# Kernel tuning notes

Measured on AMD Instinct MI355X. Metric: run time of the kernel, lower is better.

Reference implementation:

```python
import jax, jax.numpy as jnp
import numpy as np

B, DIM, H, N, M = 2, 256, 4, 4096, 4096
DH = DIM // H  # per-head dim
EPS = 1e-5


def conv1(x, W, b):
    # kernel_size=1 Conv1d == channel-wise linear: x [B,Cin,N], W [Cin,Cout]
    return jnp.einsum('bin,io->bon', x, W) + b[None, :, None]


def setup_inputs() -> dict:
    key = jax.random.key(0)
    ks = jax.random.split(key, 12)
    s = lambda fan: 1.0 / np.sqrt(fan)
    return {
        'x': jax.random.normal(ks[0], (B, DIM, N), jnp.float32),
        'source': jax.random.normal(ks[1], (B, DIM, M), jnp.float32),
        'Wq': jax.random.normal(ks[2], (DIM, DIM), jnp.float32) * s(DIM),
        'bq': jax.random.normal(ks[3], (DIM,), jnp.float32) * 0.01,
        'Wk': jax.random.normal(ks[4], (DIM, DIM), jnp.float32) * s(DIM),
        'bk': jax.random.normal(ks[5], (DIM,), jnp.float32) * 0.01,
        'Wv': jax.random.normal(ks[6], (DIM, DIM), jnp.float32) * s(DIM),
        'bv': jax.random.normal(ks[7], (DIM,), jnp.float32) * 0.01,
        'Wo': jax.random.normal(ks[8], (DIM, DIM), jnp.float32) * s(DIM),
        'bo': jax.random.normal(ks[9], (DIM,), jnp.float32) * 0.01,
        'W1': jax.random.normal(ks[10], (2 * DIM, 2 * DIM), jnp.float32) * s(2 * DIM),
        'b1': jnp.zeros((2 * DIM,), jnp.float32),
        'gamma': jnp.ones((2 * DIM,), jnp.float32),
        'beta': jnp.zeros((2 * DIM,), jnp.float32),
        'W2': jax.random.normal(ks[11], (2 * DIM, DIM), jnp.float32) * s(2 * DIM),
        'b2': jnp.zeros((DIM,), jnp.float32),
    }


def reference(x, source, Wq, bq, Wk, bk, Wv, bv, Wo, bo, W1, b1, gamma, beta, W2, b2):
    b = x.shape[0]
    # projections, then split channels as (d_head, heads): view(B, DH, H, L)
    q = conv1(x, Wq, bq).reshape(b, DH, H, -1)       # [B,DH,H,N]
    k = conv1(source, Wk, bk).reshape(b, DH, H, -1)  # [B,DH,H,M]
    v = conv1(source, Wv, bv).reshape(b, DH, H, -1)  # [B,DH,H,M]
    scores = jnp.einsum('bdhn,bdhm->bhnm', q, k) / np.sqrt(DH)  # [B,H,N,M]
    p = jax.nn.softmax(scores, axis=-1)
    attn = jnp.einsum('bhnm,bdhm->bdhn', p, v)        # [B,DH,H,N]
    message = conv1(attn.reshape(b, DIM, -1), Wo, bo)  # [B,DIM,N]
    h = conv1(jnp.concatenate([x, message], axis=1), W1, b1)  # [B,2DIM,N]
    # BatchNorm1d in train mode: batch stats over (batch, length)
    mean = jnp.mean(h, axis=(0, 2), keepdims=True)
    var = jnp.var(h, axis=(0, 2), keepdims=True)
    h = (h - mean) * jax.lax.rsqrt(var + EPS)
    h = h * gamma[None, :, None] + beta[None, :, None]
    h = jax.nn.relu(h)
    return conv1(h, W2, b2)  # [B,DIM,N]
```

## Files before the change

### kernel.cpp

```cpp
#include <hip/hip_runtime.h>
#include <hip/hip_bf16.h>
#include <math.h>

#define NB   2
#define DIM  256
#define NH   4
#define DH   64
#define LEN  4096
#define EPSBN 1e-5f
#define QSC  0.18033688f

typedef __attribute__((ext_vector_type(8))) short bf16x8;
typedef __attribute__((ext_vector_type(4))) float f32x4;
typedef __attribute__((ext_vector_type(16))) float f32x16;
typedef __attribute__((ext_vector_type(4))) unsigned short u16x4;
typedef unsigned short ushortT;

__device__ __forceinline__ unsigned short f2bf(float f) {
    unsigned int u = __float_as_uint(f);
    u += 0x7FFFu + ((u >> 16) & 1u);
    return (unsigned short)(u >> 16);
}
__device__ __forceinline__ float bf2f(unsigned short u) {
    return __uint_as_float(((unsigned int)u) << 16);
}
__device__ __forceinline__ unsigned int cvtpk_bf16(float lo, float hi) {
    unsigned int r;
    asm volatile("v_cvt_pk_bf16_f32 %0, %1, %2" : "=v"(r) : "v"(lo), "v"(hi));
    return r;
}
__device__ __forceinline__ float sum16(const f32x16& v) {
    float s01 = v[0] + v[1], s23 = v[2] + v[3], s45 = v[4] + v[5], s67 = v[6] + v[7];
    float s89 = v[8] + v[9], sab = v[10] + v[11], scd = v[12] + v[13], sef = v[14] + v[15];
    return ((s01 + s23) + (s45 + s67)) + ((s89 + sab) + (scd + sef));
}
#define MFMA(a, b, c)   __builtin_amdgcn_mfma_f32_16x16x32_bf16((a), (b), (c), 0, 0, 0)
#define MFMA32(a, b, c) __builtin_amdgcn_mfma_f32_32x32x16_bf16((a), (b), (c), 0, 0, 0)

__global__ __launch_bounds__(256)
void prep_all(const float* __restrict__ x, const float* __restrict__ src,
              const float* __restrict__ Wq, const float* __restrict__ Wk,
              const float* __restrict__ Wv, const float* __restrict__ Wo,
              const float* __restrict__ W1, const float* __restrict__ W2,
              const float* __restrict__ bq, const float* __restrict__ bk,
              const float* __restrict__ bv, const float* __restrict__ bo,
              const float* __restrict__ b1v,
              ushortT* WqT, ushortT* WkT, ushortT* WvT,
              ushortT* W1fT, ushortT* W2T,
              float* bqs, float* bks, float* bvs, float* bfused,
              ushortT* __restrict__ xT, ushortT* __restrict__ srcT)
{
    const int y = blockIdx.y;
    const int idx = blockIdx.x * 256 + threadIdx.x;
    const int t = threadIdx.x;
    if (y <= 2) {
        if (idx < 65536) {
            int op = idx >> 8, i = idx & 255;
            int o = (op & 63) * 4 + (op >> 6);
            if (y == 0)      WqT[idx] = f2bf(Wq[i * 256 + o] * QSC);
            else if (y == 1) WkT[idx] = f2bf(Wk[i * 256 + o]);
            else             WvT[idx] = f2bf(Wv[i * 256 + o]);
        }
    } else if (y == 3) {
        int o = idx >> 9, i = idx & 511;
        if (i < 256) W1fT[o * 512 + i] = f2bf(W1[i * 512 + o]);
    } else if (y == 4) {
        if (idx < 131072) { int o = idx >> 9, i = idx & 511; W2T[idx] = f2bf(W2[i * 256 + o]); }
    } else if (y == 5) {
        if (blockIdx.x == 0 && idx < 256) {
            int o = (idx & 63) * 4 + (idx >> 6);
            bqs[idx] = bq[o] * QSC;
            bks[idx] = bk[o];
            bvs[idx] = bv[o];
        }
    } else if (y <= 7) {
        const int bid = blockIdx.x + (y - 6) * 1024;
        const int c0 = (bid & 31) * 8;
        const int n0 = ((bid >> 5) & 15) * 256;
        const int z = bid >> 9;
        const int b = z & 1;
        const float* in = (z >> 1) ? src : x;
        ushortT* out = (z >> 1) ? srcT : xT;
        const int n = n0 + t;
        bf16x8 v;
#pragma unroll
        for (int j = 0; j < 8; ++j)
            v[j] = (short)f2bf(in[(((b << 8) + c0 + j) << 12) + n]);
        *(bf16x8*)&out[(((b << 12) + n) << 8) + c0] = v;
    } else {
        if (blockIdx.x >= 40) return;
        const int oy = blockIdx.x / 5, xi = blockIdx.x % 5;
        __shared__ float red[4][64];
        if (xi == 4) {
            const int part = t >> 6, oo = t & 63;
            const int o = oy * 64 + oo;
            float s = 0.f;
            for (int c = part * 64; c < part * 64 + 64; ++c)
                s += bo[c] * W1[(256 + c) * 512 + o];
            red[part][oo] = s;
            __syncthreads();
            if (part == 0)
                bfused[o] = ((red[0][oo] + red[1][oo]) + (red[2][oo] + red[3][oo])) + b1v[o];
            return;
        }
        const int w = t >> 6, l2 = t & 63, lg = l2 >> 4, ll = l2 & 15;
        const int wr = w >> 1, wc = w & 1;
        const int a0t = xi * 64, o0 = oy * 64;
        const int oA = o0 + wr * 32;
        const int aB = a0t + wc * 32;
        f32x4 acc[2][2] = {};
        const int ra = aB + ll, rb = aB + 16 + ll;
        const int r0 = (ra & 63) * 4 + (ra >> 6);
        const int r1 = (rb & 63) * 4 + (rb >> 6);
#pragma unroll
        for (int kk = 0; kk < 256; kk += 32) {
            const int cbase = 256 + kk + lg * 8;
            bf16x8 a0, a1;
#pragma unroll
            for (int j = 0; j < 8; ++j) {
                a0[j] = (short)f2bf(W1[(size_t)(cbase + j) * 512 + oA + ll]);
                a1[j] = (short)f2bf(W1[(size_t)(cbase + j) * 512 + oA + 16 + ll]);
            }
            const float* p0 = Wo + r0 * 256 + kk + lg * 8;
            const float* p1 = Wo + r1 * 256 + kk + lg * 8;
            float4 f00 = *(const float4*)p0, f01 = *(const float4*)(p0 + 4);
            float4 f10 = *(const float4*)p1, f11 = *(const float4*)(p1 + 4);
            bf16x8 b0, b1;
            b0[0] = (short)f2bf(f00.x); b0[1] = (short)f2bf(f00.y);
            b0[2] = (short)f2bf(f00.z); b0[3] = (short)f2bf(f00.w);
            b0[4] = (short)f2bf(f01.x); b0[5] = (short)f2bf(f01.y);
            b0[6] = (short)f2bf(f01.z); b0[7] = (short)f2bf(f01.w);
            b1[0] = (short)f2bf(f10.x); b1[1] = (short)f2bf(f10.y);
            b1[2] = (short)f2bf(f10.z); b1[3] = (short)f2bf(f10.w);
            b1[4] = (short)f2bf(f11.x); b1[5] = (short)f2bf(f11.y);
            b1[6] = (short)f2bf(f11.z); b1[7] = (short)f2bf(f11.w);
            acc[0][0] = MFMA(a0, b0, acc[0][0]);
            acc[0][1] = MFMA(a0, b1, acc[0][1]);
            acc[1][0] = MFMA(a1, b0, acc[1][0]);
            acc[1][1] = MFMA(a1, b1, acc[1][1]);
        }
#pragma unroll
        for (int f = 0; f < 2; ++f)
#pragma unroll
            for (int g = 0; g < 2; ++g) {
                const int ap = aB + g * 16 + ll;
#pragma unroll
                for (int r = 0; r < 4; ++r) {
                    const int o = oA + f * 16 + lg * 4 + r;
                    W1fT[o * 512 + 256 + ap] = f2bf(acc[f][g][r]);
                }
            }
    }
}

#define GEMM_STAGE(AROWP, BROWP)                                              \
    {                                                                         \
        _Pragma("unroll")                                                     \
        for (int i_ = 0; i_ < 4; ++i_) {                                      \
            const int row_ = i_ * 32 + srow;                                  \
            bf16x8 va_ = *(const bf16x8*)(AROWP(row_) + sc8 * 8);             \
            bf16x8 vb_ = *(const bf16x8*)(BROWP(row_) + sc8 * 8);             \
            const int dst_ = (row_ * 8 + (sc8 ^ (row_ & 7))) * 8;             \
            *(bf16x8*)&ldsA[dst_] = va_;                                      \
            *(bf16x8*)&ldsB[dst_] = vb_;                                      \
        }                                                                     \
    }

#define GEMM_FRAGS(k2_)                                                       \
    bf16x8 af[4], bfr[4];                                                     \
    {                                                                         \
        _Pragma("unroll")                                                     \
        for (int fo_ = 0; fo_ < 4; ++fo_) {                                   \
            const int ra_ = wr * 64 + fo_ * 16 + ll;                          \
            af[fo_] = *(const bf16x8*)&ldsA[(ra_ * 8 + (((k2_) * 4 + lg) ^ (ra_ & 7))) * 8]; \
            const int rb_ = wc * 64 + fo_ * 16 + ll;                          \
            bfr[fo_] = *(const bf16x8*)&ldsB[(rb_ * 8 + (((k2_) * 4 + lg) ^ (rb_ & 7))) * 8]; \
        }                                                                     \
    }

#define GEMM_MFMA16()                                                         \
    _Pragma("unroll")                                                         \
    for (int fo_ = 0; fo_ < 4; ++fo_) {                                       \
        _Pragma("unroll")                                                     \
        for (int fn_ = 0; fn_ < 4; ++fn_)                                     \
            acc[fo_][fn_] = MFMA(af[fo_], bfr[fn_], acc[fo_][fn_]);           \
    }

__global__ __launch_bounds__(256)
void qkv128(const ushortT* __restrict__ xT, const ushortT* __restrict__ srcT,
            const ushortT* __restrict__ WqT, const ushortT* __restrict__ WkT,
            const ushortT* __restrict__ WvT,
            const float* __restrict__ bqs, const float* __restrict__ bks,
            const float* __restrict__ bvs,
            ushortT* __restrict__ QT, ushortT* __restrict__ KT,
            ushortT* __restrict__ Vb)
{
    __shared__ __align__(16) ushortT ldsA[8192];
    __shared__ __align__(16) ushortT ldsB[8192];
    const int z = blockIdx.z, sel = z >> 1, b = z & 1;
    const int t = threadIdx.x, w = t >> 6, l = t & 63, lg = l >> 4, ll = l & 15;
    const int wr = w >> 1, wc = w & 1;
    const int n0 = blockIdx.x * 128, o0 = blockIdx.y * 128;
    const int srow = t >> 3, sc8 = t & 7;

    const ushortT* Agl;
    const ushortT* Bgl;
    int Arb, Brb;
    if (sel == 0)      { Agl = WqT;  Arb = o0;              Bgl = xT;   Brb = (b << 12) + n0; }
    else if (sel == 1) { Agl = WkT;  Arb = o0;              Bgl = srcT; Brb = (b << 12) + n0; }
    else               { Agl = srcT; Arb = (b << 12) + n0;  Bgl = WvT;  Brb = o0; }

    f32x4 acc[4][4] = {};
#define AROW(r_) (Agl + (size_t)(Arb + (r_)) * 256 + kk)
#define BROW(r_) (Bgl + (size_t)(Brb + (r_)) * 256 + kk)
    for (int kk = 0; kk < 256; kk += 64) {
        GEMM_STAGE(AROW, BROW);
        __syncthreads();
#pragma unroll
        for (int k2 = 0; k2 < 2; ++k2) {
            GEMM_FRAGS(k2);
            GEMM_MFMA16();
        }
        __syncthreads();
    }
#undef AROW
#undef BROW

    if (sel < 2) {
        const float* bias = sel ? bks : bqs;
        ushortT* out = sel ? KT : QT;
#pragma unroll
        for (int f = 0; f < 4; ++f) {
            const int ob = o0 + wr * 64 + f * 16 + lg * 4;
            f32x4 bv = *(const f32x4*)&bias[ob];
            const int hh = ob >> 6, d = ob & 63;
#pragma unroll
            for (int g = 0; g < 4; ++g) {
                const int n = n0 + wc * 64 + g * 16 + ll;
                u16x4 pk;
#pragma unroll
                for (int r = 0; r < 4; ++r) pk[r] = f2bf(acc[f][g][r] + bv[r]);
                *(u16x4*)&out[((((b << 2) + hh) << 12) + n) * 64 + d] = pk;
            }
        }
    } else {
#pragma unroll
        for (int g = 0; g < 4; ++g) {
            const int op = o0 + wc * 64 + g * 16 + ll;
            const float bb = bvs[op];
            const int hh = op >> 6, d = op & 63;
#pragma unroll
            for (int f = 0; f < 4; ++f) {
                const int m = n0 + wr * 64 + f * 16 + lg * 4;
                u16x4 pk;
#pragma unroll
                for (int r = 0; r < 4; ++r) pk[r] = f2bf(acc[f][g][r] + bb);
                *(u16x4*)&Vb[((((b << 2) + hh) << 6) + d) * 4096 + m] = pk;
            }
        }
    }
}

__global__ __launch_bounds__(256)
void gemmh128(const ushortT* __restrict__ xT, const ushortT* __restrict__ attnT,
              const ushortT* __restrict__ W1fT, const float* __restrict__ bfused,
              ushortT* __restrict__ hT, float* __restrict__ Sp, float* __restrict__ SSp)
{
    __shared__ __align__(16) ushortT ldsA[8192];
    __shared__ __align__(16) ushortT ldsB[8192];
    const int t = threadIdx.x, w = t >> 6, l = t & 63, lg = l >> 4, ll = l & 15;
    const int wr = w >> 1, wc = w & 1;
    const int n0 = blockIdx.x * 128, o0 = blockIdx.y * 128, b = blockIdx.z;
    const int srow = t >> 3, sc8 = t & 7;

    f32x4 acc[4][4] = {};
    for (int kk = 0; kk < 512; kk += 64) {
        const ushortT* Bsrc = (kk < 256) ? xT : attnT;
        const int kb = kk & 255;
#define AROW(r_) (W1fT + (size_t)(o0 + (r_)) * 512 + kk)
#define BROW(r_) (Bsrc + (size_t)((b << 12) + n0 + (r_)) * 256 + kb)
        GEMM_STAGE(AROW, BROW);
#undef AROW
#undef BROW
        __syncthreads();
#pragma unroll
        for (int k2 = 0; k2 < 2; ++k2) {
            GEMM_FRAGS(k2);
            GEMM_MFMA16();
        }
        __syncthreads();
    }

#pragma unroll
    for (int f = 0; f < 4; ++f) {
        const int ob = o0 + wr * 64 + f * 16 + lg * 4;
        f32x4 bv = *(const f32x4*)&bfused[ob];
        f32x4 hv[4];
#pragma unroll
        for (int g = 0; g < 4; ++g) {
            const int n = n0 + wc * 64 + g * 16 + ll;
            u16x4 pk;
#pragma unroll
            for (int r = 0; r < 4; ++r) {
                hv[g][r] = acc[f][g][r] + bv[r];
                pk[r] = f2bf(hv[g][r]);
            }
            *(u16x4*)&hT[(((b << 12) + n) << 9) + ob] = pk;
        }
#pragma unroll
        for (int r = 0; r < 4; ++r) {
            float s  = (hv[0][r] + hv[1][r]) + (hv[2][r] + hv[3][r]);
            float q2 = (hv[0][r] * hv[0][r] + hv[1][r] * hv[1][r]) +
                       (hv[2][r] * hv[2][r] + hv[3][r] * hv[3][r]);
#pragma unroll
            for (int off = 1; off < 16; off <<= 1) {
                s  += __shfl_xor(s, off);
                q2 += __shfl_xor(q2, off);
            }
            if (ll == 0) {
                const int o = ob + r;
                const int pidx = (o * 2 + b) * 64 + blockIdx.x * 2 + wc;
                Sp[pidx] = s;
                SSp[pidx] = q2;
            }
        }
    }
}

__global__ __launch_bounds__(128)
void bn_fin2(const float* __restrict__ S, const float* __restrict__ SS,
             const float* __restrict__ gamma, const float* __restrict__ beta,
             float* __restrict__ scale, float* __restrict__ shift)
{
    const int c = blockIdx.x, t = threadIdx.x;
    float s = S[c * 128 + t];
    float ss = SS[c * 128 + t];
#pragma unroll
    for (int off = 32; off; off >>= 1) {
        s += __shfl_down(s, off);
        ss += __shfl_down(ss, off);
    }
    __shared__ float red[4];
    const int wid = t >> 6;
    if ((t & 63) == 0) { red[wid] = s; red[2 + wid] = ss; }
    __syncthreads();
    if (t == 0) {
        s = red[0] + red[1];
        ss = red[2] + red[3];
        const float cnt = (float)NB * (float)LEN;
        float mean = s / cnt;
        float var = ss / cnt - mean * mean;
        float sc = gamma[c] * rsqrtf(var + EPSBN);
        scale[c] = sc;
        shift[c] = beta[c] - mean * sc;
    }
}

__global__ __launch_bounds__(256)
void gemmw2_128(const ushortT* __restrict__ hT, const ushortT* __restrict__ W2T,
                const float* __restrict__ bias, const float* __restrict__ scale,
                const float* __restrict__ shift, float* __restrict__ out)
{
    __shared__ __align__(16) ushortT ldsA[8192];
    __shared__ __align__(16) ushortT ldsB[8192];
    const int t = threadIdx.x, w = t >> 6, l = t & 63, lg = l >> 4, ll = l & 15;
    const int wr = w >> 1, wc = w & 1;
    const int n0 = blockIdx.x * 128, o0 = blockIdx.y * 128, b = blockIdx.z;
    const int srow = t >> 3, sc8 = t & 7;

    f32x4 acc[4][4] = {};
    for (int kk = 0; kk < 512; kk += 64) {
#define AROW(r_) (W2T + (size_t)(o0 + (r_)) * 512 + kk)
#define BROW(r_) (hT + (size_t)((b << 12) + n0 + (r_)) * 512 + kk)
        GEMM_STAGE(AROW, BROW);
#undef AROW
#undef BROW
        __syncthreads();
#pragma unroll
        for (int k2 = 0; k2 < 2; ++k2) {
            GEMM_FRAGS(k2);
            const int ch = kk + k2 * 32 + lg * 8;
            f32x4 sc0 = *(const f32x4*)&scale[ch];
            f32x4 sc1 = *(const f32x4*)&scale[ch + 4];
            f32x4 sh0 = *(const f32x4*)&shift[ch];
            f32x4 sh1 = *(const f32x4*)&shift[ch + 4];
#pragma unroll
            for (int fn = 0; fn < 4; ++fn) {
                bf16x8 raw = bfr[fn], bb;
#pragma unroll
                for (int j = 0; j < 4; ++j) {
                    float v0 = fmaxf(bf2f((unsigned short)raw[j]) * sc0[j] + sh0[j], 0.f);
                    float v1 = fmaxf(bf2f((unsigned short)raw[j + 4]) * sc1[j] + sh1[j], 0.f);
                    bb[j] = (short)f2bf(v0);
                    bb[j + 4] = (short)f2bf(v1);
                }
                bfr[fn] = bb;
            }
            GEMM_MFMA16();
        }
        __syncthreads();
    }

#pragma unroll
    for (int f = 0; f < 4; ++f) {
        const int ob = o0 + wr * 64 + f * 16 + lg * 4;
        f32x4 bv = *(const f32x4*)&bias[ob];
#pragma unroll
        for (int g = 0; g < 4; ++g) {
            const int n = n0 + wc * 64 + g * 16 + ll;
#pragma unroll
            for (int r = 0; r < 4; ++r)
                out[(((b << 8) + ob + r) << 12) + n] = acc[f][g][r] + bv[r];
        }
    }
}

__global__ __launch_bounds__(256)
void attn9(const ushortT* __restrict__ QT, const ushortT* __restrict__ KT,
           const ushortT* __restrict__ Vg, ushortT* __restrict__ attnT)
{
    __shared__ __align__(16) float olds[6144];
    __shared__ float llds[192];
    const int t = threadIdx.x, w = t >> 6, l = t & 63;
    const int hi = l >> 5, ln = l & 31;
    const int f = blockIdx.x, bh = f & 7, nt = f >> 3;
    const int b = bh >> 2, h = bh & 3;
    const int n0 = nt * 64;

    bf16x8 qf[2][4];
#pragma unroll
    for (int qb = 0; qb < 2; ++qb) {
        const int qrow = ((bh << 12) + n0 + qb * 32 + ln) * 64 + hi * 8;
#pragma unroll
        for (int dblk = 0; dblk < 4; ++dblk)
            qf[qb][dblk] = *(const bf16x8*)&QT[qrow + dblk * 16];
    }

    f32x16 o[2][2] = {};
    float l_loc[2] = {0.f, 0.f};

    const ushortT* Kb0 = KT + ((bh << 12) + w * 32 + ln) * 64 + hi * 8;
    const ushortT* Vb0 = Vg + ((bh << 6) + ln) * 4096 + w * 32 + hi * 8;

#pragma unroll 1
    for (int s = 0; s < 32; ++s) {
        const ushortT* Kp = Kb0 + s * 128 * 64;
        f32x16 st0 = {}, st1 = {};
        {
            bf16x8 ka = *(const bf16x8*)(Kp);
            bf16x8 kb = *(const bf16x8*)(Kp + 16);
            __builtin_amdgcn_s_setprio(1);
            st0 = MFMA32(ka, qf[0][0], st0);
            st1 = MFMA32(ka, qf[1][0], st1);
            st0 = MFMA32(kb, qf[0][1], st0);
            st1 = MFMA32(kb, qf[1][1], st1);
            __builtin_amdgcn_s_setprio(0);
            ka = *(const bf16x8*)(Kp + 32);
            kb = *(const bf16x8*)(Kp + 48);
            __builtin_amdgcn_s_setprio(1);
            st0 = MFMA32(ka, qf[0][2], st0);
            st1 = MFMA32(ka, qf[1][2], st1);
            st0 = MFMA32(kb, qf[0][3], st0);
            st1 = MFMA32(kb, qf[1][3], st1);
            __builtin_amdgcn_s_setprio(0);
        }

#pragma unroll
        for (int r = 0; r < 16; ++r) st0[r] = __builtin_amdgcn_exp2f(st0[r]);
#pragma unroll
        for (int r = 0; r < 16; ++r) st1[r] = __builtin_amdgcn_exp2f(st1[r]);
        l_loc[0] += sum16(st0);
        l_loc[1] += sum16(st1);

        bf16x8 pb0[2], pb1[2];
        {
            unsigned int pk0[8], pk1[8];
#pragma unroll
            for (int j = 0; j < 8; ++j) {
                pk0[j] = cvtpk_bf16(st0[2 * j], st0[2 * j + 1]);
                pk1[j] = cvtpk_bf16(st1[2 * j], st1[2 * j + 1]);
            }
#pragma unroll
            for (int sb = 0; sb < 2; ++sb) {
                unsigned int a0 = pk0[4 * sb], b0 = pk0[4 * sb + 2];
                unsigned int a1 = pk0[4 * sb + 1], b1 = pk0[4 * sb + 3];
                asm volatile("v_permlane32_swap_b32 %0, %1" : "+v"(a0), "+v"(b0));
                asm volatile("v_permlane32_swap_b32 %0, %1" : "+v"(a1), "+v"(b1));
                union { unsigned int u[4]; bf16x8 v; } tp;
                tp.u[0] = a0; tp.u[1] = a1; tp.u[2] = b0; tp.u[3] = b1;
                pb0[sb] = tp.v;
                unsigned int c0 = pk1[4 * sb], d0 = pk1[4 * sb + 2];
                unsigned int c1 = pk1[4 * sb + 1], d1 = pk1[4 * sb + 3];
                asm volatile("v_permlane32_swap_b32 %0, %1" : "+v"(c0), "+v"(d0));
                asm volatile("v_permlane32_swap_b32 %0, %1" : "+v"(c1), "+v"(d1));
                union { unsigned int u[4]; bf16x8 v; } tq;
                tq.u[0] = c0; tq.u[1] = c1; tq.u[2] = d0; tq.u[3] = d1;
                pb1[sb] = tq.v;
            }
        }

        const ushortT* Vp = Vb0 + s * 128;
        {
            bf16x8 va = *(const bf16x8*)(Vp);
            bf16x8 vb = *(const bf16x8*)(Vp + 16);
            __builtin_amdgcn_s_setprio(1);
            o[0][0] = MFMA32(va, pb0[0], o[0][0]);
            o[1][0] = MFMA32(va, pb1[0], o[1][0]);
            o[0][0] = MFMA32(vb, pb0[1], o[0][0]);
            o[1][0] = MFMA32(vb, pb1[1], o[1][0]);
            __builtin_amdgcn_s_setprio(0);
            va = *(const bf16x8*)(Vp + 32 * 4096);
            vb = *(const bf16x8*)(Vp + 32 * 4096 + 16);
            __builtin_amdgcn_s_setprio(1);
            o[0][1] = MFMA32(va, pb0[0], o[0][1]);
            o[1][1] = MFMA32(va, pb1[0], o[1][1]);
            o[0][1] = MFMA32(vb, pb0[1], o[0][1]);
            o[1][1] = MFMA32(vb, pb1[1], o[1][1]);
            __builtin_amdgcn_s_setprio(0);
        }
    }

    float lw[2];
    lw[0] = l_loc[0] + __shfl_xor(l_loc[0], 32);
    lw[1] = l_loc[1] + __shfl_xor(l_loc[1], 32);
    if (w && hi == 0) {
        llds[(w - 1) * 64 + ln] = lw[0];
        llds[(w - 1) * 64 + 32 + ln] = lw[1];
    }
#pragma unroll
    for (int qb = 0; qb < 2; ++qb) {
        if (w) {
            const int base = (w - 1) * 2048 + l;
#pragma unroll
            for (int r = 0; r < 16; ++r) olds[base + r * 64] = o[qb][0][r];
#pragma unroll
            for (int r = 0; r < 16; ++r) olds[base + (16 + r) * 64] = o[qb][1][r];
        }
        __syncthreads();
        if (w == 0) {
#pragma unroll
            for (int j = 0; j < 3; ++j) {
                const int base = j * 2048 + l;
#pragma unroll
                for (int r = 0; r < 16; ++r) o[qb][0][r] += olds[base + r * 64];
#pragma unroll
                for (int r = 0; r < 16; ++r) o[qb][1][r] += olds[base + (16 + r) * 64];
            }
        }
        __syncthreads();
    }

    if (w == 0) {
        float li[2] = {lw[0], lw[1]};
#pragma unroll
        for (int j = 0; j < 3; ++j) {
            li[0] += llds[j * 64 + ln];
            li[1] += llds[j * 64 + 32 + ln];
        }
#pragma unroll
        for (int qb = 0; qb < 2; ++qb) {
            const float linv = 1.f / li[qb];
            ushortT* orow = attnT + ((((b << 12) + n0 + qb * 32 + ln)) << 8) + (h << 6);
#pragma unroll
            for (int j = 0; j < 8; ++j) {
                const int d0 = ((2 * j) & 3) + 8 * (j >> 1) + 4 * hi;
                *(unsigned int*)&orow[d0] =
                    cvtpk_bf16(o[qb][0][2 * j] * linv, o[qb][0][2 * j + 1] * linv);
                *(unsigned int*)&orow[32 + d0] =
                    cvtpk_bf16(o[qb][1][2 * j] * linv, o[qb][1][2 * j + 1] * linv);
            }
        }
    }
}

extern "C" void kernel_launch(void* const* d_in, const int* in_sizes, int n_in,
                              void* d_out, int out_size, void* d_ws, size_t ws_size,
                              hipStream_t stream)
{
    const float* x   = (const float*)d_in[0];
    const float* src = (const float*)d_in[1];
    const float* Wq  = (const float*)d_in[2];
    const float* bq  = (const float*)d_in[3];
    const float* Wk  = (const float*)d_in[4];
    const float* bk  = (const float*)d_in[5];
    const float* Wv  = (const float*)d_in[6];
    const float* bv  = (const float*)d_in[7];
    const float* Wo  = (const float*)d_in[8];
    const float* bo  = (const float*)d_in[9];
    const float* W1  = (const float*)d_in[10];
    const float* b1  = (const float*)d_in[11];
    const float* gam = (const float*)d_in[12];
    const float* bet = (const float*)d_in[13];
    const float* W2  = (const float*)d_in[14];
    const float* b2  = (const float*)d_in[15];
    float* outp = (float*)d_out;

    char* W = (char*)d_ws;
    ushortT* xT    = (ushortT*)(W);
    ushortT* srcT  = (ushortT*)(W + (4u << 20));
    ushortT* QT    = (ushortT*)(W + (8u << 20));
    ushortT* KT    = (ushortT*)(W + (12u << 20));
    ushortT* Vb    = (ushortT*)(W + (16u << 20));
    ushortT* attnT = (ushortT*)(W + (20u << 20));
    ushortT* hT    = KT;
    float* Sp  = (float*)(W + (8u << 20));
    float* SSp = (float*)(W + (9u << 20));
    char* WB = W + (24u << 20);
    ushortT* WqT  = (ushortT*)(WB);
    ushortT* WkT  = (ushortT*)(WB + (128u << 10));
    ushortT* WvT  = (ushortT*)(WB + (256u << 10));
    ushortT* W1fT = (ushortT*)(WB + (640u << 10));
    ushortT* W2T  = (ushortT*)(WB + (1152u << 10));
    float* bqs    = (float*)(WB + (1408u << 10));
    float* bks    = (float*)(WB + (1409u << 10));
    float* bvs    = (float*)(WB + (1410u << 10));
    float* bfused = (float*)(WB + (1412u << 10));
    float* scl    = (float*)(WB + (1416u << 10));
    float* sft    = (float*)(WB + (1418u << 10));

    prep_all<<<dim3(1024, 9), 256, 0, stream>>>(x, src, Wq, Wk, Wv, Wo, W1, W2,
                                                bq, bk, bv, bo, b1,
                                                WqT, WkT, WvT, W1fT, W2T,
                                                bqs, bks, bvs, bfused, xT, srcT);

    qkv128<<<dim3(32, 2, 6), 256, 0, stream>>>(xT, srcT, WqT, WkT, WvT,
                                               bqs, bks, bvs, QT, KT, Vb);

    attn9<<<dim3(512), dim3(256), 0, stream>>>(QT, KT, Vb, attnT);

    gemmh128<<<dim3(32, 4, 2), 256, 0, stream>>>(xT, attnT, W1fT, bfused, hT, Sp, SSp);

    bn_fin2<<<dim3(512), 128, 0, stream>>>(Sp, SSp, gam, bet, scl, sft);

    gemmw2_128<<<dim3(32, 2, 2), 256, 0, stream>>>(hT, W2T, b2, scl, sft, outp);
}
```

Before: 152.9 us.

## Software-pipeline attention loop: overlap next QK^T MFMA with current softmax

Restructures the attention main loop into a two-stage software pipeline, unrolled by two. K tiles are prefetched two steps ahead, and the QK^T MFMAs for the next tile are issued before the exp2/pack/PV of the current tile. The aim is to hide global load latency and overlap MFMA work with the VALU softmax. The cost is higher register pressure from extra in-flight K/V fragments and score tiles, which could lower occupancy or cause spills.

Measured after the change: 155.7 us. About the same (+1.9%).

```diff
diff --git a/kernel.cpp b/kernel.cpp
--- a/kernel.cpp
+++ b/kernel.cpp
@@ -415,9 +415,84 @@
     }
 }
 
+struct KF { bf16x8 a, b, c, d; };
+
+__device__ __forceinline__ KF loadK(const ushortT* p) {
+    KF k;
+    k.a = *(const bf16x8*)(p);
+    k.b = *(const bf16x8*)(p + 16);
+    k.c = *(const bf16x8*)(p + 32);
+    k.d = *(const bf16x8*)(p + 48);
+    return k;
+}
+__device__ __forceinline__ KF loadV(const ushortT* p) {
+    KF v;
+    v.a = *(const bf16x8*)(p);
+    v.b = *(const bf16x8*)(p + 16);
+    v.c = *(const bf16x8*)(p + 32 * 4096);
+    v.d = *(const bf16x8*)(p + 32 * 4096 + 16);
+    return v;
+}
+__device__ __forceinline__ void qk8(const KF& k, const bf16x8 qf[2][4],
+                                    f32x16& s0, f32x16& s1) {
+    f32x16 z0 = {}, z1 = {};
+    __builtin_amdgcn_s_setprio(1);
+    z0 = MFMA32(k.a, qf[0][0], z0); z1 = MFMA32(k.a, qf[1][0], z1);
+    z0 = MFMA32(k.b, qf[0][1], z0); z1 = MFMA32(k.b, qf[1][1], z1);
+    z0 = MFMA32(k.c, qf[0][2], z0); z1 = MFMA32(k.c, qf[1][2], z1);
+    z0 = MFMA32(k.d, qf[0][3], z0); z1 = MFMA32(k.d, qf[1][3], z1);
+    __builtin_amdgcn_s_setprio(0);
+    s0 = z0; s1 = z1;
+}
+__device__ __forceinline__ void smax(f32x16& s0, f32x16& s1,
+                                     bf16x8* pb0, bf16x8* pb1, float* l_loc) {
+#pragma unroll
+    for (int r = 0; r < 16; ++r) s0[r] = __builtin_amdgcn_exp2f(s0[r]);
+#pragma unroll
+    for (int r = 0; r < 16; ++r) s1[r] = __builtin_amdgcn_exp2f(s1[r]);
+    l_loc[0] += sum16(s0);
+    l_loc[1] += sum16(s1);
+    unsigned int pk0[8], pk1[8];
+#pragma unroll
+    for (int j = 0; j < 8; ++j) {
+        pk0[j] = cvtpk_bf16(s0[2 * j], s0[2 * j + 1]);
+        pk1[j] = cvtpk_bf16(s1[2 * j], s1[2 * j + 1]);
+    }
+#pragma unroll
+    for (int sb = 0; sb < 2; ++sb) {
+        unsigned int a0 = pk0[4 * sb], b0 = pk0[4 * sb + 2];
+        unsigned int a1 = pk0[4 * sb + 1], b1 = pk0[4 * sb + 3];
+        asm volatile("v_permlane32_swap_b32 %0, %1" : "+v"(a0), "+v"(b0));
+        asm volatile("v_permlane32_swap_b32 %0, %1" : "+v"(a1), "+v"(b1));
+        union { unsigned int u[4]; bf16x8 v; } tp;
+        tp.u[0] = a0; tp.u[1] = a1; tp.u[2] = b0; tp.u[3] = b1;
+        pb0[sb] = tp.v;
+        unsigned int c0 = pk1[4 * sb], d0 = pk1[4 * sb + 2];
+        unsigned int c1 = pk1[4 * sb + 1], d1 = pk1[4 * sb + 3];
+        asm volatile("v_permlane32_swap_b32 %0, %1" : "+v"(c0), "+v"(d0));
+        asm volatile("v_permlane32_swap_b32 %0, %1" : "+v"(c1), "+v"(d1));
+        union { unsigned int u[4]; bf16x8 v; } tq;
+        tq.u[0] = c0; tq.u[1] = c1; tq.u[2] = d0; tq.u[3] = d1;
+        pb1[sb] = tq.v;
+    }
+}
+__device__ __forceinline__ void pv8(const KF& v, const bf16x8* pb0,
+                                    const bf16x8* pb1, f32x16 o[2][2]) {
+    __builtin_amdgcn_s_setprio(1);
+    o[0][0] = MFMA32(v.a, pb0[0], o[0][0]);
+    o[1][0] = MFMA32(v.a, pb1[0], o[1][0]);
+    o[0][0] = MFMA32(v.b, pb0[1], o[0][0]);
+    o[1][0] = MFMA32(v.b, pb1[1], o[1][0]);
+    o[0][1] = MFMA32(v.c, pb0[0], o[0][1]);
+    o[1][1] = MFMA32(v.c, pb1[0], o[1][1]);
+    o[0][1] = MFMA32(v.d, pb0[1], o[0][1]);
+    o[1][1] = MFMA32(v.d, pb1[1], o[1][1]);
+    __builtin_amdgcn_s_setprio(0);
+}
+
 __global__ __launch_bounds__(256)
-void attn9(const ushortT* __restrict__ QT, const ushortT* __restrict__ KT,
-           const ushortT* __restrict__ Vg, ushortT* __restrict__ attnT)
+void attn11(const ushortT* __restrict__ QT, const ushortT* __restrict__ KT,
+            const ushortT* __restrict__ Vg, ushortT* __restrict__ attnT)
 {
     __shared__ __align__(16) float olds[6144];
     __shared__ float llds[192];
@@ -441,84 +516,34 @@
 
     const ushortT* Kb0 = KT + ((bh << 12) + w * 32 + ln) * 64 + hi * 8;
     const ushortT* Vb0 = Vg + ((bh << 6) + ln) * 4096 + w * 32 + hi * 8;
+#define KSTEP (128 * 64)
+
+    KF kt = loadK(Kb0);
+    KF kB = loadK(Kb0 + KSTEP);
+    f32x16 stA0, stA1;
+    qk8(kt, qf, stA0, stA1);
 
 #pragma unroll 1
-    for (int s = 0; s < 32; ++s) {
-        const ushortT* Kp = Kb0 + s * 128 * 64;
-        f32x16 st0 = {}, st1 = {};
+    for (int s = 0; s < 32; s += 2) {
         {
-            bf16x8 ka = *(const bf16x8*)(Kp);
-            bf16x8 kb = *(const bf16x8*)(Kp + 16);
-            __builtin_amdgcn_s_setprio(1);
-            st0 = MFMA32(ka, qf[0][0], st0);
-            st1 = MFMA32(ka, qf[1][0], st1);
-            st0 = MFMA32(kb, qf[0][1], st0);
-            st1 = MFMA32(kb, qf[1][1], st1);
-            __builtin_amdgcn_s_setprio(0);
-            ka = *(const bf16x8*)(Kp + 32);
-            kb = *(const bf16x8*)(Kp + 48);
-            __builtin_amdgcn_s_setprio(1);
-            st0 = MFMA32(ka, qf[0][2], st0);
-            st1 = MFMA32(ka, qf[1][2], st1);
-            st0 = MFMA32(kb, qf[0][3], st0);
-            st1 = MFMA32(kb, qf[1][3], st1);
-            __builtin_amdgcn_s_setprio(0);
-        }
-
-#pragma unroll
-        for (int r = 0; r < 16; ++r) st0[r] = __builtin_amdgcn_exp2f(st0[r]);
-#pragma unroll
-        for (int r = 0; r < 16; ++r) st1[r] = __builtin_amdgcn_exp2f(st1[r]);
-        l_loc[0] += sum16(st0);
-        l_loc[1] += sum16(st1);
-
-        bf16x8 pb0[2], pb1[2];
-        {
-            unsigned int pk0[8], pk1[8];
-#pragma unroll
-            for (int j = 0; j < 8; ++j) {
-                pk0[j] = cvtpk_bf16(st0[2 * j], st0[2 * j + 1]);
-                pk1[j] = cvtpk_bf16(st1[2 * j], st1[2 * j + 1]);
-            }
-#pragma unroll
-            for (int sb = 0; sb < 2; ++sb) {
-                unsigned int a0 = pk0[4 * sb], b0 = pk0[4 * sb + 2];
-                unsigned int a1 = pk0[4 * sb + 1], b1 = pk0[4 * sb + 3];
-                asm volatile("v_permlane32_swap_b32 %0, %1" : "+v"(a0), "+v"(b0));
-                asm volatile("v_permlane32_swap_b32 %0, %1" : "+v"(a1), "+v"(b1));
-                union { unsigned int u[4]; bf16x8 v; } tp;
-                tp.u[0] = a0; tp.u[1] = a1; tp.u[2] = b0; tp.u[3] = b1;
-                pb0[sb] = tp.v;
-                unsigned int c0 = pk1[4 * sb], d0 = pk1[4 * sb + 2];
-                unsigned int c1 = pk1[4 * sb + 1], d1 = pk1[4 * sb + 3];
-                asm volatile("v_permlane32_swap_b32 %0, %1" : "+v"(c0), "+v"(d0));
-                asm volatile("v_permlane32_swap_b32 %0, %1" : "+v"(c1), "+v"(d1));
-                union { unsigned int u[4]; bf16x8 v; } tq;
-                tq.u[0] = c0; tq.u[1] = c1; tq.u[2] = d0; tq.u[3] = d1;
-                pb1[sb] = tq.v;
-            }
-        }
-
-        const ushortT* Vp = Vb0 + s * 128;
-        {
-            bf16x8 va = *(const bf16x8*)(Vp);
-            bf16x8 vb = *(const bf16x8*)(Vp + 16);
-            __builtin_amdgcn_s_setprio(1);
-            o[0][0] = MFMA32(va, pb0[0], o[0][0]);
-            o[1][0] = MFMA32(va, pb1[0], o[1][0]);
-            o[0][0] = MFMA32(vb, pb0[1], o[0][0]);
-            o[1][0] = MFMA32(vb, pb1[1], o[1][0]);
-            __builtin_amdgcn_s_setprio(0);
-            va = *(const bf16x8*)(Vp + 32 * 4096);
-            vb = *(const bf16x8*)(Vp + 32 * 4096 + 16);
-            __builtin_amdgcn_s_setprio(1);
-            o[0][1] = MFMA32(va, pb0[0], o[0][1]);
-            o[1][1] = MFMA32(va, pb1[0], o[1][1]);
-            o[0][1] = MFMA32(vb, pb0[1], o[0][1]);
-            o[1][1] = MFMA32(vb, pb1[1], o[1][1]);
-            __builtin_amdgcn_s_setprio(0);
-        }
-    }
+            const int sk = (s + 2 < 32) ? s + 2 : 31;
+            KF kC = loadK(Kb0 + sk * KSTEP);
+            KF vA = loadV(Vb0 + s * 128);
+            f32x16 stB0, stB1;
+            qk8(kB, qf, stB0, stB1);
+            bf16x8 pA0[2], pA1[2];
+            smax(stA0, stA1, pA0, pA1, l_loc);
+            pv8(vA, pA0, pA1, o);
+            const int sk2 = (s + 3 < 32) ? s + 3 : 31;
+            kB = loadK(Kb0 + sk2 * KSTEP);
+            KF vB = loadV(Vb0 + (s + 1) * 128);
+            qk8(kC, qf, stA0, stA1);
+            bf16x8 pB0[2], pB1[2];
+            smax(stB0, stB1, pB0, pB1, l_loc);
+            pv8(vB, pB0, pB1, o);
+        }
+    }
+#undef KSTEP
 
     float lw[2];
     lw[0] = l_loc[0] + __shfl_xor(l_loc[0], 32);
@@ -626,7 +651,7 @@
     qkv128<<<dim3(32, 2, 6), 256, 0, stream>>>(xT, srcT, WqT, WkT, WvT,
                                                bqs, bks, bvs, QT, KT, Vb);
 
-    attn9<<<dim3(512), dim3(256), 0, stream>>>(QT, KT, Vb, attnT);
+    attn11<<<dim3(512), dim3(256), 0, stream>>>(QT, KT, Vb, attnT);
 
     gemmh128<<<dim3(32, 4, 2), 256, 0, stream>>>(xT, attnT, W1fT, bfused, hT, Sp, SSp);
 
```
